# Kernel tuning notes

Hardware: AMD Instinct MI355X
Metric: run time of the kernel (lower is better)

Reference implementation:

```python
import jax, jax.numpy as jnp
import numpy as np

C_IN, C_OUT, N, H, W = 128, 256, 3, 256, 256


def im2row(x, n, h, w, c):
    """x: [h*w, c] channel-last pixel-major image -> [(h-n+1)*(w-n+1), c*n*n]
    with each row ordered (channel, ki, kj) to match w.reshape(C_OUT,-1).T."""
    img = x.reshape(h, w, c)
    oh, ow = h - n + 1, w - n + 1
    # stack the n*n shifted views; last axis index = ki*n + kj
    patches = jnp.stack(
        [img[ki:ki + oh, kj:kj + ow, :] for ki in range(n) for kj in range(n)],
        axis=-1,
    )  # [oh, ow, c, n*n]
    return patches.reshape(oh * ow, c * n * n)


def setup_inputs() -> dict:
    key = jax.random.key(0)
    k1, k2, k3, k4 = jax.random.split(key, 4)
    x = jax.random.normal(k1, (H * W, C_IN), dtype=jnp.float32)
    # pre-quantized int8 kernel values (stored as int32), symmetric range
    kernel_q = jax.random.randint(k2, (C_IN * N * N, C_OUT), -127, 128, dtype=jnp.int32)
    kernel_scale = jax.random.uniform(k3, (1,), dtype=jnp.float32, minval=1e-3, maxval=1e-2)
    bias = jax.random.normal(k4, (C_OUT,), dtype=jnp.float32)
    return {"x": x, "kernel_q": kernel_q, "kernel_scale": kernel_scale, "bias": bias}


def reference(x, kernel_q, kernel_scale, bias):
    # im2row unfolding (irregular gather)
    rows = im2row(x, N, H, W, C_IN)                      # [OH*OW, C_IN*N*N]
    # int8 quantized matmul (weights dequantized by per-tensor scale) + bias
    acc = rows @ kernel_q.astype(jnp.float32)            # [OH*OW, C_OUT]
    return acc * kernel_scale + bias
```

## Files before the change

kernel.cpp:

```cpp
#include <hip/hip_runtime.h>
#include <stdint.h>

#define WW 256
#define CIN 128
#define COUT 256
#define OHW 64516
#define KTOT 1152
#define BM 256
#define BK 64
#define NSTEP 18
#define NWG 253
#define BUFSZ 65536

typedef __attribute__((ext_vector_type(8))) short short8;
typedef __attribute__((ext_vector_type(4))) float float4v;
typedef __attribute__((ext_vector_type(4))) float f32x4;
typedef __attribute__((ext_vector_type(2))) unsigned int uint2v;

__device__ __forceinline__ short f2bf(float f) {
    unsigned u = __builtin_bit_cast(unsigned, f);
    unsigned r = u + 0x7fffu + ((u >> 16) & 1u);
    return (short)(r >> 16);
}

__global__ void prep_weights(const int* __restrict__ kq, unsigned short* __restrict__ wt) {
    int o  = blockIdx.x * 256 + threadIdx.x;
    int co = o / KTOT;
    int kp = o - co * KTOT;
    int q  = kp >> 7;
    int c  = kp & 127;
    wt[o] = (unsigned short)f2bf((float)kq[(c * 9 + q) * 256 + co]);
}

__device__ __forceinline__ void gload16(const void* g, void* l) {
    __builtin_amdgcn_global_load_lds(
        (const __attribute__((address_space(1))) unsigned int*)g,
        (__attribute__((address_space(3))) unsigned int*)l, 16, 0, 0);
}

__device__ __forceinline__ unsigned cvtpk(float lo, float hi) {
    unsigned r;
    asm("v_cvt_pk_bf16_f32 %0, %1, %2" : "=v"(r) : "v"(lo), "v"(hi));
    return r;
}

#define SB  __builtin_amdgcn_sched_barrier(0)
#define BAR __builtin_amdgcn_s_barrier()
#define WAIT_VM(n) asm volatile("s_waitcnt vmcnt(" #n ")" ::: "memory")
#define WAIT_LGKM  asm volatile("s_waitcnt lgkmcnt(0)" ::: "memory")

__global__ __launch_bounds__(512, 2) void conv_gemm(
    const float* __restrict__ x,
    const unsigned short* __restrict__ wt,
    const float* __restrict__ scale_p,
    const float* __restrict__ bias,
    float* __restrict__ out)
{
    __shared__ __align__(16) char lds[2 * BUFSZ];

    const int tid  = threadIdx.x;
    const int lane = tid & 63;
    const int wave = tid >> 6;

    const int orig = blockIdx.x;
    const int xcd  = orig & 7;
    const int idx8 = orig >> 3;
    const int wg   = (xcd < 5 ? xcd * 32 : 160 + (xcd - 5) * 31) + idx8;
    const int pbase = wg * BM;

    const int acol16 = tid & 15;
    const int arow0  = tid >> 4;
    int arowbase[8];
#pragma unroll
    for (int r = 0; r < 8; ++r) {
        int p = pbase + arow0 + r * 32;
        if (p > OHW - 1) p = OHW - 1;
        int oy = p / 254;
        int ox = p - oy * 254;
        arowbase[r] = (oy * WW + ox) * CIN;
    }
    const int aswz  = (arow0 & 7) << 4;
    const int adst0 = arow0 * 128 + ((acol16 * 8) ^ aswz);

    int bsrc[4];
#pragma unroll
    for (int it = 0; it < 4; ++it) {
        int z    = it * 8192 + wave * 1024 + lane * 16;
        int co   = z >> 7;
        int colb = (z & 127) ^ ((co & 7) << 4);
        bsrc[it] = co * KTOT + (colb >> 1);
    }

    const int wr128 = (wave >> 2) * 128;
    const int wc64  = (wave & 3) * 64;
    const int llo   = lane & 15;
    const int lhi16 = (lane >> 4) * 16;

    f32x4 acc[8][4];
#pragma unroll
    for (int m = 0; m < 8; m++)
#pragma unroll
        for (int n = 0; n < 4; n++) acc[m][n] = (f32x4)0.f;

    float4v fr[8];
    short8  af[4], bfr[4];

#define ISSUE_A(lo_, tk) do {                                                   \
    int q_ = (tk) >> 1;  int ki_ = q_ / 3;  int kj_ = q_ - ki_ * 3;             \
    int aoff = (ki_ * WW + kj_) * CIN + (((tk) & 1) << 6) + acol16 * 4;         \
    _Pragma("unroll")                                                           \
    for (int r = (lo_); r < (lo_) + 4; ++r)                                     \
        fr[r] = *(const float4v*)(x + arowbase[r] + aoff);                      \
} while (0)

#define WRITE_A(bufb, lo_) do {                                                 \
    _Pragma("unroll")                                                           \
    for (int r = (lo_); r < (lo_) + 4; ++r) {                                   \
        uint2v U;                                                               \
        U.x = cvtpk(fr[r][0], fr[r][1]);                                        \
        U.y = cvtpk(fr[r][2], fr[r][3]);                                        \
        *(uint2v*)(lds + (bufb) + adst0 + r * 4096) = U;                        \
    }                                                                           \
} while (0)

#define GLOAD_B(bufb, tk) do {                                                  \
    _Pragma("unroll")                                                           \
    for (int it = 0; it < 4; ++it)                                              \
        gload16(wt + bsrc[it] + (tk) * 64,                                      \
                lds + (bufb) + 32768 + it * 8192 + wave * 1024);                \
} while (0)

#define READ_B(bufb, kk) do {                                                   \
    _Pragma("unroll")                                                           \
    for (int n = 0; n < 4; ++n) {                                               \
        int co  = wc64 + n * 16 + llo;                                          \
        int off = co * 128 + (((kk) * 64 + lhi16) ^ ((co & 7) << 4));           \
        bfr[n] = *(const short8*)(lds + (bufb) + 32768 + off);                  \
    }                                                                           \
} while (0)

#define READ_A(bufb, mh, kk) do {                                               \
    _Pragma("unroll")                                                           \
    for (int mi = 0; mi < 4; ++mi) {                                            \
        int row = wr128 + (mh) * 64 + mi * 16 + llo;                            \
        int off = row * 128 + (((kk) * 64 + lhi16) ^ ((row & 7) << 4));         \
        af[mi] = *(const short8*)(lds + (bufb) + off);                          \
    }                                                                           \
} while (0)

#define MFMA16(mh) do {                                                         \
    __builtin_amdgcn_s_setprio(1);                                              \
    _Pragma("unroll")                                                           \
    for (int mi = 0; mi < 4; ++mi)                                              \
        _Pragma("unroll")                                                       \
        for (int n = 0; n < 4; ++n)                                             \
            acc[(mh) * 4 + mi][n] = __builtin_amdgcn_mfma_f32_16x16x32_bf16(    \
                af[mi], bfr[n], acc[(mh) * 4 + mi][n], 0, 0, 0);                \
    __builtin_amdgcn_s_setprio(0);                                              \
} while (0)

#define TILE(CUR, NXT, TK1, DOSTAGE) do {                                       \
                                                           \
    READ_B(CUR, 0); READ_A(CUR, 0, 0);                                          \
    if (DOSTAGE) { GLOAD_B(NXT, TK1); ISSUE_A(0, TK1); }                        \
    SB; BAR; WAIT_LGKM; SB; MFMA16(0); SB; BAR; SB;                             \
                                                           \
    READ_A(CUR, 1, 0);                                                          \
    if (DOSTAGE) { ISSUE_A(4, TK1); }                                           \
    SB; BAR; WAIT_LGKM; SB; MFMA16(1); SB; BAR; SB;                             \
                                                           \
    READ_B(CUR, 1); READ_A(CUR, 0, 1);                                          \
    if (DOSTAGE) { WAIT_VM(4); WRITE_A(NXT, 0); }                               \
    SB; BAR; WAIT_LGKM; SB; MFMA16(0); SB; BAR; SB;                             \
                                                           \
    READ_A(CUR, 1, 1);                                                          \
    if (DOSTAGE) { WAIT_VM(0); WRITE_A(NXT, 4); }                               \
    SB; BAR; WAIT_LGKM; SB; MFMA16(1); SB; BAR; SB;                             \
} while (0)

    GLOAD_B(0, 0);
    ISSUE_A(0, 0);
    ISSUE_A(4, 0);
    WAIT_VM(0);
    WRITE_A(0, 0);
    WRITE_A(0, 4);
    WAIT_LGKM; SB; BAR; SB;

#pragma unroll 2
    for (int t = 0; t < 16; t += 2) {
        TILE(0,     BUFSZ, t + 1, 1);
        TILE(BUFSZ, 0,     t + 2, 1);
    }
    TILE(0,     BUFSZ, 17, 1);
    TILE(BUFSZ, 0,     0,  0);

    const float scl = scale_p[0];
    const int lhi4 = (lane >> 4) * 4;
    float bv[4];
#pragma unroll
    for (int n = 0; n < 4; ++n) bv[n] = bias[wc64 + n * 16 + llo];
#pragma unroll
    for (int m = 0; m < 8; ++m) {
#pragma unroll
        for (int r = 0; r < 4; ++r) {
            const int pp = pbase + wr128 + m * 16 + lhi4 + r;
            if (pp < OHW) {
#pragma unroll
                for (int n = 0; n < 4; ++n)
                    out[pp * COUT + wc64 + n * 16 + llo] = acc[m][n][r] * scl + bv[n];
            }
        }
    }
#undef ISSUE_A
#undef WRITE_A
#undef GLOAD_B
#undef READ_B
#undef READ_A
#undef MFMA16
#undef TILE
}

extern "C" void kernel_launch(void* const* d_in, const int* in_sizes, int n_in,
                              void* d_out, int out_size, void* d_ws, size_t ws_size,
                              hipStream_t stream) {
    const float* x     = (const float*)d_in[0];
    const int*   kq    = (const int*)d_in[1];
    const float* scale = (const float*)d_in[2];
    const float* bias  = (const float*)d_in[3];
    float*       out   = (float*)d_out;
    unsigned short* wt = (unsigned short*)d_ws;

    prep_weights<<<KTOT, 256, 0, stream>>>(kq, wt);
    conv_gemm<<<NWG, 512, 0, stream>>>(x, wt, scale, bias, out);
}
```

Baseline: 137.6 us.

## Shrink GEMM tile to 128x128 with 256-thread workgroups and N split

Result: no change. 140.0 us (+1.7%).

```diff
diff --git a/kernel.cpp b/kernel.cpp
--- a/kernel.cpp
+++ b/kernel.cpp
@@ -6,11 +6,12 @@
 #define COUT 256
 #define OHW 64516
 #define KTOT 1152
-#define BM 256
+#define BM 128
+#define BN 128
 #define BK 64
 #define NSTEP 18
-#define NWG 253
-#define BUFSZ 65536
+#define NWG 1010
+#define BUFSZ 32768
 
 typedef __attribute__((ext_vector_type(8))) short short8;
 typedef __attribute__((ext_vector_type(4))) float float4v;
@@ -49,7 +50,7 @@
 #define WAIT_VM(n) asm volatile("s_waitcnt vmcnt(" #n ")" ::: "memory")
 #define WAIT_LGKM  asm volatile("s_waitcnt lgkmcnt(0)" ::: "memory")
 
-__global__ __launch_bounds__(512, 2) void conv_gemm(
+__global__ __launch_bounds__(256, 2) void conv_gemm(
     const float* __restrict__ x,
     const unsigned short* __restrict__ wt,
     const float* __restrict__ scale_p,
@@ -65,15 +66,18 @@
     const int orig = blockIdx.x;
     const int xcd  = orig & 7;
     const int idx8 = orig >> 3;
-    const int wg   = (xcd < 5 ? xcd * 32 : 160 + (xcd - 5) * 31) + idx8;
-    const int pbase = wg * BM;
+    const int wg   = (xcd < 2 ? xcd * 127 : 254 + (xcd - 2) * 126) + idx8;
+    const int mblk = wg >> 1;
+    const int nblk = wg & 1;
+    const int pbase = mblk * BM;
+    const int co0   = nblk * BN;
 
     const int acol16 = tid & 15;
     const int arow0  = tid >> 4;
     int arowbase[8];
 #pragma unroll
     for (int r = 0; r < 8; ++r) {
-        int p = pbase + arow0 + r * 32;
+        int p = pbase + r * 16 + arow0;
         if (p > OHW - 1) p = OHW - 1;
         int oy = p / 254;
         int ox = p - oy * 254;
@@ -85,41 +89,41 @@
     int bsrc[4];
 #pragma unroll
     for (int it = 0; it < 4; ++it) {
-        int z    = it * 8192 + wave * 1024 + lane * 16;
+        int z    = it * 4096 + wave * 1024 + lane * 16;
         int co   = z >> 7;
         int colb = (z & 127) ^ ((co & 7) << 4);
-        bsrc[it] = co * KTOT + (colb >> 1);
-    }
-
-    const int wr128 = (wave >> 2) * 128;
-    const int wc64  = (wave & 3) * 64;
+        bsrc[it] = (co0 + co) * KTOT + (colb >> 1);
+    }
+
+    const int wr64  = (wave >> 1) * 64;
+    const int wc64  = (wave & 1) * 64;
     const int llo   = lane & 15;
     const int lhi16 = (lane >> 4) * 16;
 
-    f32x4 acc[8][4];
-#pragma unroll
-    for (int m = 0; m < 8; m++)
+    f32x4 acc[4][4];
+#pragma unroll
+    for (int m = 0; m < 4; m++)
 #pragma unroll
         for (int n = 0; n < 4; n++) acc[m][n] = (f32x4)0.f;
 
     float4v fr[8];
     short8  af[4], bfr[4];
 
-#define ISSUE_A(lo_, tk) do {                                                   \
+#define ISSUE_A(tk) do {                                                        \
     int q_ = (tk) >> 1;  int ki_ = q_ / 3;  int kj_ = q_ - ki_ * 3;             \
     int aoff = (ki_ * WW + kj_) * CIN + (((tk) & 1) << 6) + acol16 * 4;         \
     _Pragma("unroll")                                                           \
-    for (int r = (lo_); r < (lo_) + 4; ++r)                                     \
+    for (int r = 0; r < 8; ++r)                                                 \
         fr[r] = *(const float4v*)(x + arowbase[r] + aoff);                      \
 } while (0)
 
-#define WRITE_A(bufb, lo_) do {                                                 \
-    _Pragma("unroll")                                                           \
-    for (int r = (lo_); r < (lo_) + 4; ++r) {                                   \
+#define WRITE_A(bufb) do {                                                      \
+    _Pragma("unroll")                                                           \
+    for (int r = 0; r < 8; ++r) {                                               \
         uint2v U;                                                               \
         U.x = cvtpk(fr[r][0], fr[r][1]);                                        \
         U.y = cvtpk(fr[r][2], fr[r][3]);                                        \
-        *(uint2v*)(lds + (bufb) + adst0 + r * 4096) = U;                        \
+        *(uint2v*)(lds + (bufb) + adst0 + r * 2048) = U;                        \
     }                                                                           \
 } while (0)
 
@@ -127,7 +131,7 @@
     _Pragma("unroll")                                                           \
     for (int it = 0; it < 4; ++it)                                              \
         gload16(wt + bsrc[it] + (tk) * 64,                                      \
-                lds + (bufb) + 32768 + it * 8192 + wave * 1024);                \
+                lds + (bufb) + 16384 + it * 4096 + wave * 1024);                \
 } while (0)
 
 #define READ_B(bufb, kk) do {                                                   \
@@ -135,56 +139,50 @@
     for (int n = 0; n < 4; ++n) {                                               \
         int co  = wc64 + n * 16 + llo;                                          \
         int off = co * 128 + (((kk) * 64 + lhi16) ^ ((co & 7) << 4));           \
-        bfr[n] = *(const short8*)(lds + (bufb) + 32768 + off);                  \
+        bfr[n] = *(const short8*)(lds + (bufb) + 16384 + off);                  \
     }                                                                           \
 } while (0)
 
-#define READ_A(bufb, mh, kk) do {                                               \
+#define READ_A(bufb, kk) do {                                                   \
     _Pragma("unroll")                                                           \
     for (int mi = 0; mi < 4; ++mi) {                                            \
-        int row = wr128 + (mh) * 64 + mi * 16 + llo;                            \
+        int row = wr64 + mi * 16 + llo;                                         \
         int off = row * 128 + (((kk) * 64 + lhi16) ^ ((row & 7) << 4));         \
         af[mi] = *(const short8*)(lds + (bufb) + off);                          \
     }                                                                           \
 } while (0)
 
-#define MFMA16(mh) do {                                                         \
+#define MFMA16() do {                                                           \
     __builtin_amdgcn_s_setprio(1);                                              \
     _Pragma("unroll")                                                           \
     for (int mi = 0; mi < 4; ++mi)                                              \
         _Pragma("unroll")                                                       \
         for (int n = 0; n < 4; ++n)                                             \
-            acc[(mh) * 4 + mi][n] = __builtin_amdgcn_mfma_f32_16x16x32_bf16(    \
-                af[mi], bfr[n], acc[(mh) * 4 + mi][n], 0, 0, 0);                \
+            acc[mi][n] = __builtin_amdgcn_mfma_f32_16x16x32_bf16(               \
+                af[mi], bfr[n], acc[mi][n], 0, 0, 0);                           \
     __builtin_amdgcn_s_setprio(0);                                              \
 } while (0)
 
 #define TILE(CUR, NXT, TK1, DOSTAGE) do {                                       \
-                                                           \
-    READ_B(CUR, 0); READ_A(CUR, 0, 0);                                          \
-    if (DOSTAGE) { GLOAD_B(NXT, TK1); ISSUE_A(0, TK1); }                        \
-    SB; BAR; WAIT_LGKM; SB; MFMA16(0); SB; BAR; SB;                             \
-                                                           \
-    READ_A(CUR, 1, 0);                                                          \
-    if (DOSTAGE) { ISSUE_A(4, TK1); }                                           \
-    SB; BAR; WAIT_LGKM; SB; MFMA16(1); SB; BAR; SB;                             \
-                                                           \
-    READ_B(CUR, 1); READ_A(CUR, 0, 1);                                          \
-    if (DOSTAGE) { WAIT_VM(4); WRITE_A(NXT, 0); }                               \
-    SB; BAR; WAIT_LGKM; SB; MFMA16(0); SB; BAR; SB;                             \
-                                                           \
-    READ_A(CUR, 1, 1);                                                          \
-    if (DOSTAGE) { WAIT_VM(0); WRITE_A(NXT, 4); }                               \
-    SB; BAR; WAIT_LGKM; SB; MFMA16(1); SB; BAR; SB;                             \
-} while (0)
-
+    if (DOSTAGE) { ISSUE_A(TK1); GLOAD_B(NXT, TK1); }                           \
+                                                                       \
+    READ_A(CUR, 0); READ_B(CUR, 0);                                             \
+    SB; BAR; WAIT_LGKM; SB; MFMA16(); SB; BAR; SB;                              \
+                                                                       \
+    READ_A(CUR, 1); READ_B(CUR, 1);                                             \
+    if (DOSTAGE) { WAIT_VM(4); WRITE_A(NXT); }                                  \
+    SB; BAR; WAIT_LGKM; SB; MFMA16(); SB;                                       \
+    if (DOSTAGE) { WAIT_VM(0); }                                                \
+    BAR; SB;                                                                    \
+} while (0)
+
+    ISSUE_A(0);
     GLOAD_B(0, 0);
-    ISSUE_A(0, 0);
-    ISSUE_A(4, 0);
+    WAIT_VM(4);
+    WRITE_A(0);
     WAIT_VM(0);
-    WRITE_A(0, 0);
-    WRITE_A(0, 4);
-    WAIT_LGKM; SB; BAR; SB;
+    WAIT_LGKM;
+    SB; BAR; SB;
 
 #pragma unroll 2
     for (int t = 0; t < 16; t += 2) {
@@ -198,16 +196,16 @@
     const int lhi4 = (lane >> 4) * 4;
     float bv[4];
 #pragma unroll
-    for (int n = 0; n < 4; ++n) bv[n] = bias[wc64 + n * 16 + llo];
-#pragma unroll
-    for (int m = 0; m < 8; ++m) {
+    for (int n = 0; n < 4; ++n) bv[n] = bias[co0 + wc64 + n * 16 + llo];
+#pragma unroll
+    for (int m = 0; m < 4; ++m) {
 #pragma unroll
         for (int r = 0; r < 4; ++r) {
-            const int pp = pbase + wr128 + m * 16 + lhi4 + r;
+            const int pp = pbase + wr64 + m * 16 + lhi4 + r;
             if (pp < OHW) {
 #pragma unroll
                 for (int n = 0; n < 4; ++n)
-                    out[pp * COUT + wc64 + n * 16 + llo] = acc[m][n][r] * scl + bv[n];
+                    out[pp * COUT + co0 + wc64 + n * 16 + llo] = acc[m][n][r] * scl + bv[n];
             }
         }
     }
@@ -231,5 +229,5 @@
     unsigned short* wt = (unsigned short*)d_ws;
 
     prep_weights<<<KTOT, 256, 0, stream>>>(kq, wt);
-    conv_gemm<<<NWG, 512, 0, stream>>>(x, wt, scale, bias, out);
-}
+    conv_gemm<<<NWG, 256, 0, stream>>>(x, wt, scale, bias, out);
+}
```

## Pre-convert input to bf16 and stream A tiles via direct global-to-LDS loads

Applied to the files above, without the earlier changes.

Result: faster. 131.8 us (-4.2%).

```diff
diff --git a/kernel.cpp b/kernel.cpp
--- a/kernel.cpp
+++ b/kernel.cpp
@@ -6,11 +6,7 @@
 #define COUT 256
 #define OHW 64516
 #define KTOT 1152
-#define BM 256
-#define BK 64
 #define NSTEP 18
-#define NWG 253
-#define BUFSZ 65536
 
 typedef __attribute__((ext_vector_type(8))) short short8;
 typedef __attribute__((ext_vector_type(4))) float float4v;
@@ -32,6 +28,16 @@
     wt[o] = (unsigned short)f2bf((float)kq[(c * 9 + q) * 256 + co]);
 }
 
+__global__ void cvt_x(const float* __restrict__ x, unsigned short* __restrict__ xb) {
+    int i = blockIdx.x * 256 + threadIdx.x;
+    float4v a = ((const float4v*)x)[i * 2];
+    float4v b = ((const float4v*)x)[i * 2 + 1];
+    short8 r;
+    r[0]=f2bf(a[0]); r[1]=f2bf(a[1]); r[2]=f2bf(a[2]); r[3]=f2bf(a[3]);
+    r[4]=f2bf(b[0]); r[5]=f2bf(b[1]); r[6]=f2bf(b[2]); r[7]=f2bf(b[3]);
+    ((short8*)xb)[i] = r;
+}
+
 __device__ __forceinline__ void gload16(const void* g, void* l) {
     __builtin_amdgcn_global_load_lds(
         (const __attribute__((address_space(1))) unsigned int*)g,
@@ -49,24 +55,168 @@
 #define WAIT_VM(n) asm volatile("s_waitcnt vmcnt(" #n ")" ::: "memory")
 #define WAIT_LGKM  asm volatile("s_waitcnt lgkmcnt(0)" ::: "memory")
 
-__global__ __launch_bounds__(512, 2) void conv_gemm(
+__global__ __launch_bounds__(512, 2) void conv_gemm_bf(
+    const unsigned short* __restrict__ xb,
+    const unsigned short* __restrict__ wt,
+    const float* __restrict__ scale_p,
+    const float* __restrict__ bias,
+    float* __restrict__ out)
+{
+    __shared__ __align__(16) char lds[2 * 65536];
+
+    const int tid  = threadIdx.x;
+    const int lane = tid & 63;
+    const int wave = tid >> 6;
+
+    const int orig = blockIdx.x;
+    const int xcd  = orig & 7;
+    const int idx8 = orig >> 3;
+    const int wg   = (xcd < 5 ? xcd * 32 : 160 + (xcd - 5) * 31) + idx8;
+    const int pbase = wg * 256;
+
+    int asrc[4];
+    int bsrc[4];
+#pragma unroll
+    for (int it = 0; it < 4; ++it) {
+        int z    = it * 8192 + tid * 16;
+        int row  = z >> 7;
+        int colb = (z & 127) ^ ((row & 7) << 4);
+        int p    = pbase + row;
+        if (p > OHW - 1) p = OHW - 1;
+        int oy = p / 254;
+        int ox = p - oy * 254;
+        asrc[it] = (oy * WW + ox) * CIN + (colb >> 1);
+        bsrc[it] = row * KTOT + (colb >> 1);
+    }
+
+    const int wr128 = (wave >> 2) * 128;
+    const int wc64  = (wave & 3) * 64;
+    const int llo   = lane & 15;
+    const int lhi16 = (lane >> 4) * 16;
+
+    f32x4 acc[8][4];
+#pragma unroll
+    for (int m = 0; m < 8; m++)
+#pragma unroll
+        for (int n = 0; n < 4; n++) acc[m][n] = (f32x4)0.f;
+
+    short8 af[4], bfr[4];
+
+#define AOFF(tk) (((((tk) >> 1) / 3) * WW + (((tk) >> 1) % 3)) * CIN + (((tk) & 1) << 6))
+
+#define GLOAD_A1(bufb, tk, it) \
+    gload16(xb + asrc[it] + AOFF(tk), lds + (bufb) + (it) * 8192 + tid * 16)
+
+#define GLOAD_B1(bufb, tk, it) \
+    gload16(wt + bsrc[it] + (tk) * 64, lds + (bufb) + 32768 + (it) * 8192 + tid * 16)
+
+#define READ_B(bufb, kk) do {                                                   \
+    _Pragma("unroll")                                                           \
+    for (int n = 0; n < 4; ++n) {                                               \
+        int co  = wc64 + n * 16 + llo;                                          \
+        int off = co * 128 + (((kk) * 64 + lhi16) ^ ((co & 7) << 4));           \
+        bfr[n] = *(const short8*)(lds + (bufb) + 32768 + off);                  \
+    }                                                                           \
+} while (0)
+
+#define READ_A(bufb, mh, kk) do {                                               \
+    _Pragma("unroll")                                                           \
+    for (int mi = 0; mi < 4; ++mi) {                                            \
+        int row = wr128 + (mh) * 64 + mi * 16 + llo;                            \
+        int off = row * 128 + (((kk) * 64 + lhi16) ^ ((row & 7) << 4));         \
+        af[mi] = *(const short8*)(lds + (bufb) + off);                          \
+    }                                                                           \
+} while (0)
+
+#define MFMA16(mh) do {                                                         \
+    __builtin_amdgcn_s_setprio(1);                                              \
+    _Pragma("unroll")                                                           \
+    for (int mi = 0; mi < 4; ++mi)                                              \
+        _Pragma("unroll")                                                       \
+        for (int n = 0; n < 4; ++n)                                             \
+            acc[(mh) * 4 + mi][n] = __builtin_amdgcn_mfma_f32_16x16x32_bf16(    \
+                af[mi], bfr[n], acc[(mh) * 4 + mi][n], 0, 0, 0);                \
+    __builtin_amdgcn_s_setprio(0);                                              \
+} while (0)
+
+#define TILE(CUR, NXT, TK1, DOSTAGE) do {                                       \
+                                                            \
+    READ_B(CUR, 0); READ_A(CUR, 0, 0);                                          \
+    if (DOSTAGE) { GLOAD_B1(NXT, TK1, 0); GLOAD_B1(NXT, TK1, 1); }              \
+    SB; BAR; WAIT_LGKM; SB; MFMA16(0); SB;                                      \
+    if (DOSTAGE) { WAIT_VM(2); } else { WAIT_VM(0); }                           \
+    BAR; SB;                                                                    \
+                                                            \
+    READ_A(CUR, 1, 0);                                                          \
+    if (DOSTAGE) { GLOAD_B1(NXT, TK1, 2); GLOAD_B1(NXT, TK1, 3); }              \
+    SB; BAR; WAIT_LGKM; SB; MFMA16(1); SB; BAR; SB;                             \
+                                                            \
+    READ_B(CUR, 1); READ_A(CUR, 0, 1);                                          \
+    if (DOSTAGE) { GLOAD_A1(NXT, TK1, 0); GLOAD_A1(NXT, TK1, 2); }              \
+    SB; BAR; WAIT_LGKM; SB; MFMA16(0); SB; BAR; SB;                             \
+                                                            \
+    READ_A(CUR, 1, 1);                                                          \
+    if (DOSTAGE) { GLOAD_A1(NXT, TK1, 1); GLOAD_A1(NXT, TK1, 3); }              \
+    SB; BAR; WAIT_LGKM; SB; MFMA16(1); SB;                                      \
+    WAIT_VM(2);                                                                 \
+    BAR; SB;                                                                    \
+} while (0)
+
+    GLOAD_B1(0, 0, 0); GLOAD_B1(0, 0, 1); GLOAD_B1(0, 0, 2); GLOAD_B1(0, 0, 3);
+    GLOAD_A1(0, 0, 0); GLOAD_A1(0, 0, 2); GLOAD_A1(0, 0, 1); GLOAD_A1(0, 0, 3);
+    WAIT_VM(0);
+    SB; BAR; SB;
+
+#pragma unroll 2
+    for (int t = 0; t < 16; t += 2) {
+        TILE(0,     65536, t + 1, 1);
+        TILE(65536, 0,     t + 2, 1);
+    }
+    TILE(0,     65536, 17, 1);
+    TILE(65536, 0,     0,  0);
+
+    const float scl = scale_p[0];
+    const int lhi4 = (lane >> 4) * 4;
+    float bv[4];
+#pragma unroll
+    for (int n = 0; n < 4; ++n) bv[n] = bias[wc64 + n * 16 + llo];
+#pragma unroll
+    for (int m = 0; m < 8; ++m) {
+#pragma unroll
+        for (int r = 0; r < 4; ++r) {
+            const int pp = pbase + wr128 + m * 16 + lhi4 + r;
+            if (pp < OHW) {
+#pragma unroll
+                for (int n = 0; n < 4; ++n)
+                    out[pp * COUT + wc64 + n * 16 + llo] = acc[m][n][r] * scl + bv[n];
+            }
+        }
+    }
+#undef GLOAD_A1
+#undef GLOAD_B1
+#undef READ_B
+#undef READ_A
+#undef MFMA16
+#undef TILE
+#undef AOFF
+}
+
+__global__ __launch_bounds__(512, 2) void conv_gemm_f32(
     const float* __restrict__ x,
     const unsigned short* __restrict__ wt,
     const float* __restrict__ scale_p,
     const float* __restrict__ bias,
     float* __restrict__ out)
 {
-    __shared__ __align__(16) char lds[2 * BUFSZ];
-
+    __shared__ __align__(16) char lds[2 * 65536];
     const int tid  = threadIdx.x;
     const int lane = tid & 63;
     const int wave = tid >> 6;
-
     const int orig = blockIdx.x;
     const int xcd  = orig & 7;
     const int idx8 = orig >> 3;
     const int wg   = (xcd < 5 ? xcd * 32 : 160 + (xcd - 5) * 31) + idx8;
-    const int pbase = wg * BM;
+    const int pbase = wg * 256;
 
     const int acol16 = tid & 15;
     const int arow0  = tid >> 4;
@@ -90,7 +240,6 @@
         int colb = (z & 127) ^ ((co & 7) << 4);
         bsrc[it] = co * KTOT + (colb >> 1);
     }
-
     const int wr128 = (wave >> 2) * 128;
     const int wc64  = (wave & 3) * 64;
     const int llo   = lane & 15;
@@ -101,7 +250,6 @@
     for (int m = 0; m < 8; m++)
 #pragma unroll
         for (int n = 0; n < 4; n++) acc[m][n] = (f32x4)0.f;
-
     float4v fr[8];
     short8  af[4], bfr[4];
 
@@ -112,7 +260,6 @@
     for (int r = (lo_); r < (lo_) + 4; ++r)                                     \
         fr[r] = *(const float4v*)(x + arowbase[r] + aoff);                      \
 } while (0)
-
 #define WRITE_A(bufb, lo_) do {                                                 \
     _Pragma("unroll")                                                           \
     for (int r = (lo_); r < (lo_) + 4; ++r) {                                   \
@@ -122,15 +269,13 @@
         *(uint2v*)(lds + (bufb) + adst0 + r * 4096) = U;                        \
     }                                                                           \
 } while (0)
-
 #define GLOAD_B(bufb, tk) do {                                                  \
     _Pragma("unroll")                                                           \
     for (int it = 0; it < 4; ++it)                                              \
         gload16(wt + bsrc[it] + (tk) * 64,                                      \
                 lds + (bufb) + 32768 + it * 8192 + wave * 1024);                \
 } while (0)
-
-#define READ_B(bufb, kk) do {                                                   \
+#define READ_B2(bufb, kk) do {                                                  \
     _Pragma("unroll")                                                           \
     for (int n = 0; n < 4; ++n) {                                               \
         int co  = wc64 + n * 16 + llo;                                          \
@@ -138,8 +283,7 @@
         bfr[n] = *(const short8*)(lds + (bufb) + 32768 + off);                  \
     }                                                                           \
 } while (0)
-
-#define READ_A(bufb, mh, kk) do {                                               \
+#define READ_A2(bufb, mh, kk) do {                                              \
     _Pragma("unroll")                                                           \
     for (int mi = 0; mi < 4; ++mi) {                                            \
         int row = wr128 + (mh) * 64 + mi * 16 + llo;                            \
@@ -147,8 +291,7 @@
         af[mi] = *(const short8*)(lds + (bufb) + off);                          \
     }                                                                           \
 } while (0)
-
-#define MFMA16(mh) do {                                                         \
+#define MFMA16B(mh) do {                                                        \
     __builtin_amdgcn_s_setprio(1);                                              \
     _Pragma("unroll")                                                           \
     for (int mi = 0; mi < 4; ++mi)                                              \
@@ -158,24 +301,19 @@
                 af[mi], bfr[n], acc[(mh) * 4 + mi][n], 0, 0, 0);                \
     __builtin_amdgcn_s_setprio(0);                                              \
 } while (0)
-
-#define TILE(CUR, NXT, TK1, DOSTAGE) do {                                       \
-                                                           \
-    READ_B(CUR, 0); READ_A(CUR, 0, 0);                                          \
+#define TILEF(CUR, NXT, TK1, DOSTAGE) do {                                      \
+    READ_B2(CUR, 0); READ_A2(CUR, 0, 0);                                        \
     if (DOSTAGE) { GLOAD_B(NXT, TK1); ISSUE_A(0, TK1); }                        \
-    SB; BAR; WAIT_LGKM; SB; MFMA16(0); SB; BAR; SB;                             \
-                                                           \
-    READ_A(CUR, 1, 0);                                                          \
+    SB; BAR; WAIT_LGKM; SB; MFMA16B(0); SB; BAR; SB;                            \
+    READ_A2(CUR, 1, 0);                                                         \
     if (DOSTAGE) { ISSUE_A(4, TK1); }                                           \
-    SB; BAR; WAIT_LGKM; SB; MFMA16(1); SB; BAR; SB;                             \
-                                                           \
-    READ_B(CUR, 1); READ_A(CUR, 0, 1);                                          \
+    SB; BAR; WAIT_LGKM; SB; MFMA16B(1); SB; BAR; SB;                            \
+    READ_B2(CUR, 1); READ_A2(CUR, 0, 1);                                        \
     if (DOSTAGE) { WAIT_VM(4); WRITE_A(NXT, 0); }                               \
-    SB; BAR; WAIT_LGKM; SB; MFMA16(0); SB; BAR; SB;                             \
-                                                           \
-    READ_A(CUR, 1, 1);                                                          \
+    SB; BAR; WAIT_LGKM; SB; MFMA16B(0); SB; BAR; SB;                            \
+    READ_A2(CUR, 1, 1);                                                         \
     if (DOSTAGE) { WAIT_VM(0); WRITE_A(NXT, 4); }                               \
-    SB; BAR; WAIT_LGKM; SB; MFMA16(1); SB; BAR; SB;                             \
+    SB; BAR; WAIT_LGKM; SB; MFMA16B(1); SB; BAR; SB;                            \
 } while (0)
 
     GLOAD_B(0, 0);
@@ -185,14 +323,13 @@
     WRITE_A(0, 0);
     WRITE_A(0, 4);
     WAIT_LGKM; SB; BAR; SB;
-
 #pragma unroll 2
     for (int t = 0; t < 16; t += 2) {
-        TILE(0,     BUFSZ, t + 1, 1);
-        TILE(BUFSZ, 0,     t + 2, 1);
-    }
-    TILE(0,     BUFSZ, 17, 1);
-    TILE(BUFSZ, 0,     0,  0);
+        TILEF(0,     65536, t + 1, 1);
+        TILEF(65536, 0,     t + 2, 1);
+    }
+    TILEF(0,     65536, 17, 1);
+    TILEF(65536, 0,     0,  0);
 
     const float scl = scale_p[0];
     const int lhi4 = (lane >> 4) * 4;
@@ -214,10 +351,10 @@
 #undef ISSUE_A
 #undef WRITE_A
 #undef GLOAD_B
-#undef READ_B
-#undef READ_A
-#undef MFMA16
-#undef TILE
+#undef READ_B2
+#undef READ_A2
+#undef MFMA16B
+#undef TILEF
 }
 
 extern "C" void kernel_launch(void* const* d_in, const int* in_sizes, int n_in,
@@ -228,8 +365,16 @@
     const float* scale = (const float*)d_in[2];
     const float* bias  = (const float*)d_in[3];
     float*       out   = (float*)d_out;
+
     unsigned short* wt = (unsigned short*)d_ws;
+    unsigned short* xb = (unsigned short*)((char*)d_ws + 589824);
 
     prep_weights<<<KTOT, 256, 0, stream>>>(kq, wt);
-    conv_gemm<<<NWG, 512, 0, stream>>>(x, wt, scale, bias, out);
-}
+
+    if (ws_size >= (size_t)589824 + 16777216) {
+        cvt_x<<<4096, 256, 0, stream>>>(x, xb);
+        conv_gemm_bf<<<253, 512, 0, stream>>>(xb, wt, scale, bias, out);
+    } else {
+        conv_gemm_f32<<<253, 512, 0, stream>>>(x, wt, scale, bias, out);
+    }
+}
```
